# Kernel optimization log

Hardware: AMD Instinct MI355X
Metric: run time of the kernel (lower is better)

Reference implementation:

```python
import jax, jax.numpy as jnp
import numpy as np

B, F_IN, N, T = 32, 64, 512, 64


def setup_inputs() -> dict:
    key = jax.random.key(0)
    ks = jax.random.split(key, 6)
    s = 0.05  # small init scale so sigmoid/softmax stay in a sane range
    return {
        "x": jax.random.normal(ks[0], (B, F_IN, N, T), dtype=jnp.float32),
        "U1": jax.random.normal(ks[1], (N,), dtype=jnp.float32) * s,
        "U2": jax.random.normal(ks[2], (N, F_IN), dtype=jnp.float32) * s,
        "U3": jax.random.normal(ks[3], (F_IN,), dtype=jnp.float32) * s,
        "be": jax.random.normal(ks[4], (1, T, T), dtype=jnp.float32) * s,
        "Ve": jax.random.normal(ks[5], (T, T), dtype=jnp.float32) * s,
    }


def reference(x, U1, U2, U3, be, Ve):
    # x: (B, F, N, T)
    # lhs = U2 @ (x^T @ U1): (B, N, T)
    t1 = jnp.einsum("bfnt,n->bft", x, U1)          # (B, F, T)
    lhs = jnp.einsum("nf,bft->bnt", U2, t1)        # (B, N, T)
    # rhs = sum_f U3[f] * x[:, f]: (B, N, T)
    rhs = jnp.einsum("f,bfnt->bnt", U3, x)         # (B, N, T)
    # product = lhs^T @ rhs: (B, T, T)
    product = jnp.einsum("bnt,bns->bts", lhs, rhs)
    # E = Ve @ sigmoid(product + be): (B, T, T)
    E = jnp.einsum("ts,bsu->btu", Ve, jax.nn.sigmoid(product + be))
    # softmax over dim=1 (rows of E), then x_flat @ A, reshape back
    A = jax.nn.softmax(E, axis=1)                  # (B, T, T)
    out = jnp.einsum("bfnt,bts->bfns", x, A)       # (B, F, N, T)
    return out
```

## Files before the change

### kernel.cpp

```cpp
#include <hip/hip_runtime.h>
#include <hip/hip_bf16.h>

#define B_ 32
#define F_ 64
#define N_ 512
#define T_ 64

typedef __attribute__((ext_vector_type(8))) short bf16x8;
typedef __attribute__((ext_vector_type(4))) float f32x4;

__device__ __forceinline__ unsigned short f2bf(float f) {
  union { float f; unsigned int u; } v; v.f = f;
  unsigned int u = v.u;
  unsigned int r = (u + 0x7FFFu + ((u >> 16) & 1u)) >> 16;
  return (unsigned short)r;
}

__device__ __forceinline__ void gl_lds16(const float* g, float* l) {
  __builtin_amdgcn_global_load_lds(
      (const __attribute__((address_space(1))) unsigned int*)(g),
      (__attribute__((address_space(3))) unsigned int*)(l),
      16, 0, 0);
}

__global__ __launch_bounds__(256) void k1_reduce(const float* __restrict__ x,
    const float* __restrict__ U1, const float* __restrict__ U3,
    float* __restrict__ t1part, float* __restrict__ rhs) {
  const int b = blockIdx.x;
  const int nc = blockIdx.y;
  const int n0 = nc * 16;
  const int tid = threadIdx.x;
  const int w = tid >> 6;
  const int lane = tid & 63;
  const int n_sub = lane >> 4;
  const int t0 = (lane & 15) * 4;

  __shared__ float ring[4][2][1024];

  const float* fbase = x + ((size_t)(b * F_ + w * 16) * N_ + n0) * T_;

  float u1c[4];
#pragma unroll
  for (int i = 0; i < 4; ++i) u1c[i] = U1[n0 + n_sub * 4 + i];

  float racc[4][4];
#pragma unroll
  for (int i = 0; i < 4; ++i)
#pragma unroll
    for (int k = 0; k < 4; ++k) racc[i][k] = 0.f;

  {
    const float* s = fbase;
    float* l = &ring[w][0][0];
#pragma unroll
    for (int c = 0; c < 4; ++c) gl_lds16(s + c * 256 + lane * 4, l + c * 256);
  }

#pragma unroll 2
  for (int j = 0; j < 16; ++j) {
    const int buf = j & 1;
    if (j < 15) {
      const float* s = fbase + (size_t)(j + 1) * (N_ * T_);
      float* l = &ring[w][buf ^ 1][0];
#pragma unroll
      for (int c = 0; c < 4; ++c) gl_lds16(s + c * 256 + lane * 4, l + c * 256);
      asm volatile("s_waitcnt vmcnt(4)" ::: "memory");
    } else {
      asm volatile("s_waitcnt vmcnt(0)" ::: "memory");
    }
    __builtin_amdgcn_sched_barrier(0);

    const int f = w * 16 + j;
    const float u3 = U3[f];
    float p0 = 0.f, p1 = 0.f, p2 = 0.f, p3 = 0.f;
#pragma unroll
    for (int i = 0; i < 4; ++i) {
      const float4 v = *(const float4*)&ring[w][buf][(n_sub * 4 + i) * 64 + t0];
      racc[i][0] += u3 * v.x; racc[i][1] += u3 * v.y;
      racc[i][2] += u3 * v.z; racc[i][3] += u3 * v.w;
      p0 += u1c[i] * v.x; p1 += u1c[i] * v.y;
      p2 += u1c[i] * v.z; p3 += u1c[i] * v.w;
    }
    p0 += __shfl_xor(p0, 16); p0 += __shfl_xor(p0, 32);
    p1 += __shfl_xor(p1, 16); p1 += __shfl_xor(p1, 32);
    p2 += __shfl_xor(p2, 16); p2 += __shfl_xor(p2, 32);
    p3 += __shfl_xor(p3, 16); p3 += __shfl_xor(p3, 32);
    if (lane < 16) {
      float4 st; st.x = p0; st.y = p1; st.z = p2; st.w = p3;
      *(float4*)&t1part[((size_t)(b * 32 + nc) * 64 + f) * 64 + t0] = st;
    }
  }

#pragma unroll
  for (int i = 0; i < 4; ++i) {
    float4 st; st.x = racc[i][0]; st.y = racc[i][1]; st.z = racc[i][2]; st.w = racc[i][3];
    *(float4*)&ring[w][0][(n_sub * 4 + i) * 64 + t0] = st;
  }
  __syncthreads();
#pragma unroll
  for (int q = 0; q < 4; ++q) {
    const int idx = q * 256 + tid;
    const float s = ring[0][0][idx] + ring[1][0][idx] + ring[2][0][idx] + ring[3][0][idx];
    rhs[((size_t)b * N_ + n0 + (idx >> 6)) * T_ + (idx & 63)] = s;
  }
}

__global__ __launch_bounds__(256) void k2_w(const float* __restrict__ rhs,
    const float* __restrict__ U2, float* __restrict__ wpart) {
  const int b = blockIdx.x;
  const int c = blockIdx.y;
  const int n0 = c * 64;
  const int tid = threadIdx.x;
  const int s = tid & 63;
  const int fg = tid >> 6;
  __shared__ float lu2[64 * 64];
  __shared__ float lr[64 * 64];
#pragma unroll
  for (int q = 0; q < 16; ++q) {
    const int idx = q * 256 + tid;
    const int i = idx >> 6, cc = idx & 63;
    lu2[idx] = U2[(size_t)(n0 + i) * F_ + cc];
    lr[idx] = rhs[((size_t)b * N_ + n0 + i) * T_ + cc];
  }
  __syncthreads();
  float acc[16];
#pragma unroll
  for (int j = 0; j < 16; ++j) acc[j] = 0.f;
  for (int i = 0; i < 64; ++i) {
    const float rv = lr[i * 64 + s];
#pragma unroll
    for (int j = 0; j < 16; ++j) acc[j] += lu2[i * 64 + fg * 16 + j] * rv;
  }
#pragma unroll
  for (int j = 0; j < 16; ++j)
    wpart[(size_t)(b * 8 + c) * 4096 + (size_t)(fg * 16 + j) * 64 + s] = acc[j];
}

__global__ __launch_bounds__(256) void kred(const float* __restrict__ t1part,
    const float* __restrict__ wpart, float* __restrict__ t1, float* __restrict__ wbf) {
  const int gid = blockIdx.x * 256 + threadIdx.x;
  if (gid < 131072) {
    const int b = gid >> 12, idx = gid & 4095;
    const float* p = t1part + (size_t)b * 32 * 4096 + idx;
    float sum = 0.f;
#pragma unroll
    for (int c = 0; c < 32; ++c) sum += p[c * 4096];
    t1[gid] = sum;
  } else {
    const int g = gid - 131072;
    const int b = g >> 12, idx = g & 4095;
    const float* p = wpart + (size_t)b * 8 * 4096 + idx;
    float sum = 0.f;
#pragma unroll
    for (int c = 0; c < 8; ++c) sum += p[c * 4096];
    wbf[g] = sum;
  }
}

__global__ __launch_bounds__(256) void k3_attn(const float* __restrict__ t1,
    const float* __restrict__ wbuf, const float* __restrict__ be,
    const float* __restrict__ Ve, float* __restrict__ Amat) {
  const int b = blockIdx.x;
  const int tid = threadIdx.x;
  const int lane = tid & 63;
  const int tg = tid >> 6;
  __shared__ float bufA[64 * 65];
  __shared__ float bufB[64 * 65];
  __shared__ float red[2][4][64];
#pragma unroll
  for (int q = 0; q < 16; ++q) {
    const int idx = q * 256 + tid;
    const int r = idx >> 6, c = idx & 63;
    bufA[r * 65 + c] = t1[(size_t)b * 4096 + idx];
    bufB[r * 65 + c] = wbuf[(size_t)b * 4096 + idx];
  }
  __syncthreads();
  float prod[16];
#pragma unroll
  for (int j = 0; j < 16; ++j) prod[j] = 0.f;
  for (int f = 0; f < 64; ++f) {
    const float wv = bufB[f * 65 + lane];
#pragma unroll
    for (int j = 0; j < 16; ++j) prod[j] += bufA[f * 65 + tg * 16 + j] * wv;
  }
  __syncthreads();
#pragma unroll
  for (int j = 0; j < 16; ++j) {
    const int tt = tg * 16 + j;
    const float v = prod[j] + be[tt * 64 + lane];
    bufA[tt * 65 + lane] = 1.f / (1.f + __expf(-v));
  }
#pragma unroll
  for (int q = 0; q < 16; ++q) {
    const int idx = q * 256 + tid;
    bufB[(idx >> 6) * 65 + (idx & 63)] = Ve[idx];
  }
  __syncthreads();
  float E[16];
#pragma unroll
  for (int j = 0; j < 16; ++j) E[j] = 0.f;
  for (int s = 0; s < 64; ++s) {
    const float sv = bufA[s * 65 + lane];
#pragma unroll
    for (int j = 0; j < 16; ++j) E[j] += bufB[(tg * 16 + j) * 65 + s] * sv;
  }
  float m = E[0];
#pragma unroll
  for (int j = 1; j < 16; ++j) m = fmaxf(m, E[j]);
  red[0][tg][lane] = m;
  __syncthreads();
  m = fmaxf(fmaxf(red[0][0][lane], red[0][1][lane]),
            fmaxf(red[0][2][lane], red[0][3][lane]));
  float se = 0.f;
  float ex[16];
#pragma unroll
  for (int j = 0; j < 16; ++j) { ex[j] = __expf(E[j] - m); se += ex[j]; }
  red[1][tg][lane] = se;
  __syncthreads();
  const float gs = red[1][0][lane] + red[1][1][lane] + red[1][2][lane] + red[1][3][lane];
  const float inv = 1.f / gs;
#pragma unroll
  for (int j = 0; j < 16; ++j) {
    const int tt = tg * 16 + j;
    Amat[(size_t)b * 4096 + tt * 64 + lane] = ex[j] * inv;
  }
}

__global__ __launch_bounds__(256) void k4_out(const float* __restrict__ x,
    const float* __restrict__ Amat, float* __restrict__ out) {
  const int b = blockIdx.x;
  const int chunk = blockIdx.y;
  const int tid = threadIdx.x;
  const int wv = tid >> 6;
  const int l = tid & 63;
  __shared__ float lA[64 * 65];
  const float* Ab = Amat + (size_t)b * 4096;
#pragma unroll
  for (int q = 0; q < 16; ++q) {
    const int idx = q * 256 + tid;
    lA[(idx >> 6) * 65 + (idx & 63)] = Ab[idx];
  }
  __syncthreads();

  const int krow0 = (l >> 4) * 8;
  const int colb = l & 15;
  bf16x8 Bf[4][2];
#pragma unroll
  for (int nt = 0; nt < 4; ++nt)
#pragma unroll
    for (int kh = 0; kh < 2; ++kh) {
      bf16x8 fr;
#pragma unroll
      for (int j = 0; j < 8; ++j) {
        const int k = kh * 32 + krow0 + j;
        fr[j] = (short)f2bf(lA[k * 65 + nt * 16 + colb]);
      }
      Bf[nt][kh] = fr;
    }

  const float* Xb = x + (size_t)b * (F_ * (size_t)N_ * T_);
  float* Ob = out + (size_t)b * (F_ * (size_t)N_ * T_);
  const int rl = l & 15;
  const int c0 = (l >> 4) * 8;

  for (int it = 0; it < 4; ++it) {
    const int tile = chunk * 16 + wv * 4 + it;
    const int r = tile * 16 + rl;
    const float* xr = Xb + (size_t)r * T_;
    const float4 v0 = *(const float4*)(xr + c0);
    const float4 v1 = *(const float4*)(xr + c0 + 4);
    const float4 v2 = *(const float4*)(xr + 32 + c0);
    const float4 v3 = *(const float4*)(xr + 32 + c0 + 4);
    bf16x8 a0, a1;
    a0[0] = (short)f2bf(v0.x); a0[1] = (short)f2bf(v0.y);
    a0[2] = (short)f2bf(v0.z); a0[3] = (short)f2bf(v0.w);
    a0[4] = (short)f2bf(v1.x); a0[5] = (short)f2bf(v1.y);
    a0[6] = (short)f2bf(v1.z); a0[7] = (short)f2bf(v1.w);
    a1[0] = (short)f2bf(v2.x); a1[1] = (short)f2bf(v2.y);
    a1[2] = (short)f2bf(v2.z); a1[3] = (short)f2bf(v2.w);
    a1[4] = (short)f2bf(v3.x); a1[5] = (short)f2bf(v3.y);
    a1[6] = (short)f2bf(v3.z); a1[7] = (short)f2bf(v3.w);

    const int rowb = tile * 16 + (l >> 4) * 4;
#pragma unroll
    for (int nt = 0; nt < 4; ++nt) {
      f32x4 c = {0.f, 0.f, 0.f, 0.f};
      c = __builtin_amdgcn_mfma_f32_16x16x32_bf16(a0, Bf[nt][0], c, 0, 0, 0);
      c = __builtin_amdgcn_mfma_f32_16x16x32_bf16(a1, Bf[nt][1], c, 0, 0, 0);
#pragma unroll
      for (int j = 0; j < 4; ++j)
        Ob[(size_t)(rowb + j) * T_ + nt * 16 + colb] = c[j];
    }
  }
}

extern "C" void kernel_launch(void* const* d_in, const int* in_sizes, int n_in,
                              void* d_out, int out_size, void* d_ws, size_t ws_size,
                              hipStream_t stream) {
  const float* x  = (const float*)d_in[0];
  const float* U1 = (const float*)d_in[1];
  const float* U2 = (const float*)d_in[2];
  const float* U3 = (const float*)d_in[3];
  const float* be = (const float*)d_in[4];
  const float* Ve = (const float*)d_in[5];
  float* out = (float*)d_out;
  float* ws = (float*)d_ws;

  float* t1part = ws;
  float* rhs    = t1part + 4194304;
  float* wpart  = rhs + 1048576;
  float* t1     = wpart + 1048576;
  float* wbf    = t1 + 131072;
  float* Amat   = wbf + 131072;

  k1_reduce<<<dim3(32, 32), 256, 0, stream>>>(x, U1, U3, t1part, rhs);
  k2_w<<<dim3(32, 8), 256, 0, stream>>>(rhs, U2, wpart);
  kred<<<1024, 256, 0, stream>>>(t1part, wpart, t1, wbf);
  k3_attn<<<32, 256, 0, stream>>>(t1, wbf, be, Ve, Amat);
  k4_out<<<dim3(32, 128), 256, 0, stream>>>(x, Amat, out);
}
```

Measured before the change: 192.9 us.

## Widen k1 node tile to 64 with 4-slot LDS ring pipeline

Each k1_reduce block now covers 64 nodes instead of 16, so the grid drops from 32x32 to 32x8 blocks and the t1 partial buffer shrinks by a factor of four. The two-slot double buffer becomes a four-slot per-wave LDS ring that keeps three 4 KB loads in flight with vmcnt(12) waits. The goal is fewer partial writes, a cheaper kred reduction and deeper memory-level parallelism. The cost is far fewer blocks (256, so the x read may under-fill the GPU), 64 KB of LDS per block and more accumulator registers, which can lower occupancy.

```diff
diff --git a/kernel.cpp b/kernel.cpp
--- a/kernel.cpp
+++ b/kernel.cpp
@@ -28,58 +28,70 @@
     float* __restrict__ t1part, float* __restrict__ rhs) {
   const int b = blockIdx.x;
   const int nc = blockIdx.y;
-  const int n0 = nc * 16;
+  const int n0 = nc * 64;
   const int tid = threadIdx.x;
   const int w = tid >> 6;
   const int lane = tid & 63;
   const int n_sub = lane >> 4;
   const int t0 = (lane & 15) * 4;
 
-  __shared__ float ring[4][2][1024];
+  __shared__ float ring[4][4][1024];
 
   const float* fbase = x + ((size_t)(b * F_ + w * 16) * N_ + n0) * T_;
 
-  float u1c[4];
-#pragma unroll
-  for (int i = 0; i < 4; ++i) u1c[i] = U1[n0 + n_sub * 4 + i];
-
-  float racc[4][4];
-#pragma unroll
-  for (int i = 0; i < 4; ++i)
-#pragma unroll
-    for (int k = 0; k < 4; ++k) racc[i][k] = 0.f;
-
-  {
-    const float* s = fbase;
-    float* l = &ring[w][0][0];
+  float u1c[4][4];
+#pragma unroll
+  for (int m = 0; m < 4; ++m)
+#pragma unroll
+    for (int i = 0; i < 4; ++i) u1c[m][i] = U1[n0 + m * 16 + n_sub * 4 + i];
+
+  float racc[4][4][4];
+#pragma unroll
+  for (int m = 0; m < 4; ++m)
+#pragma unroll
+    for (int i = 0; i < 4; ++i)
+#pragma unroll
+      for (int k = 0; k < 4; ++k) racc[m][i][k] = 0.f;
+
+#pragma unroll
+  for (int s0 = 0; s0 < 3; ++s0) {
+    const float* s = fbase + s0 * 1024;
+    float* l = &ring[w][s0][0];
 #pragma unroll
     for (int c = 0; c < 4; ++c) gl_lds16(s + c * 256 + lane * 4, l + c * 256);
   }
 
-#pragma unroll 2
   for (int j = 0; j < 16; ++j) {
-    const int buf = j & 1;
-    if (j < 15) {
-      const float* s = fbase + (size_t)(j + 1) * (N_ * T_);
-      float* l = &ring[w][buf ^ 1][0];
-#pragma unroll
-      for (int c = 0; c < 4; ++c) gl_lds16(s + c * 256 + lane * 4, l + c * 256);
-      asm volatile("s_waitcnt vmcnt(4)" ::: "memory");
-    } else {
-      asm volatile("s_waitcnt vmcnt(0)" ::: "memory");
-    }
-    __builtin_amdgcn_sched_barrier(0);
-
-    const int f = w * 16 + j;
-    const float u3 = U3[f];
+    const float u3 = U3[w * 16 + j];
     float p0 = 0.f, p1 = 0.f, p2 = 0.f, p3 = 0.f;
 #pragma unroll
-    for (int i = 0; i < 4; ++i) {
-      const float4 v = *(const float4*)&ring[w][buf][(n_sub * 4 + i) * 64 + t0];
-      racc[i][0] += u3 * v.x; racc[i][1] += u3 * v.y;
-      racc[i][2] += u3 * v.z; racc[i][3] += u3 * v.w;
-      p0 += u1c[i] * v.x; p1 += u1c[i] * v.y;
-      p2 += u1c[i] * v.z; p3 += u1c[i] * v.w;
+    for (int m = 0; m < 4; ++m) {
+      if (j < 15 || m == 0) {
+        const int fp = (m == 0) ? j : (j + 1);
+        const int mp = (m + 3) & 3;
+        const float* s = fbase + (size_t)fp * (N_ * T_) + mp * 1024;
+        float* l = &ring[w][mp][0];
+#pragma unroll
+        for (int c = 0; c < 4; ++c) gl_lds16(s + c * 256 + lane * 4, l + c * 256);
+      }
+      if (j < 15) {
+        asm volatile("s_waitcnt vmcnt(12)" ::: "memory");
+      } else {
+        if (m == 0)      asm volatile("s_waitcnt vmcnt(12)" ::: "memory");
+        else if (m == 1) asm volatile("s_waitcnt vmcnt(8)"  ::: "memory");
+        else if (m == 2) asm volatile("s_waitcnt vmcnt(4)"  ::: "memory");
+        else             asm volatile("s_waitcnt vmcnt(0)"  ::: "memory");
+      }
+      __builtin_amdgcn_sched_barrier(0);
+
+#pragma unroll
+      for (int i = 0; i < 4; ++i) {
+        const float4 v = *(const float4*)&ring[w][m][(n_sub * 4 + i) * 64 + t0];
+        racc[m][i][0] += u3 * v.x; racc[m][i][1] += u3 * v.y;
+        racc[m][i][2] += u3 * v.z; racc[m][i][3] += u3 * v.w;
+        p0 += u1c[m][i] * v.x; p1 += u1c[m][i] * v.y;
+        p2 += u1c[m][i] * v.z; p3 += u1c[m][i] * v.w;
+      }
     }
     p0 += __shfl_xor(p0, 16); p0 += __shfl_xor(p0, 32);
     p1 += __shfl_xor(p1, 16); p1 += __shfl_xor(p1, 32);
@@ -87,20 +99,24 @@
     p3 += __shfl_xor(p3, 16); p3 += __shfl_xor(p3, 32);
     if (lane < 16) {
       float4 st; st.x = p0; st.y = p1; st.z = p2; st.w = p3;
-      *(float4*)&t1part[((size_t)(b * 32 + nc) * 64 + f) * 64 + t0] = st;
-    }
-  }
-
-#pragma unroll
-  for (int i = 0; i < 4; ++i) {
-    float4 st; st.x = racc[i][0]; st.y = racc[i][1]; st.z = racc[i][2]; st.w = racc[i][3];
-    *(float4*)&ring[w][0][(n_sub * 4 + i) * 64 + t0] = st;
-  }
-  __syncthreads();
-#pragma unroll
-  for (int q = 0; q < 4; ++q) {
-    const int idx = q * 256 + tid;
-    const float s = ring[0][0][idx] + ring[1][0][idx] + ring[2][0][idx] + ring[3][0][idx];
+      *(float4*)&t1part[((size_t)(b * 8 + nc) * 64 + (w * 16 + j)) * 64 + t0] = st;
+    }
+  }
+
+#pragma unroll
+  for (int m = 0; m < 4; ++m)
+#pragma unroll
+    for (int i = 0; i < 4; ++i) {
+      float4 st; st.x = racc[m][i][0]; st.y = racc[m][i][1];
+      st.z = racc[m][i][2]; st.w = racc[m][i][3];
+      *(float4*)&ring[w][0][(m * 16 + n_sub * 4 + i) * 64 + t0] = st;
+    }
+  __syncthreads();
+  const float* r0 = &ring[0][0][0];
+#pragma unroll
+  for (int q = 0; q < 16; ++q) {
+    const int idx = q * 256 + tid;
+    const float s = r0[idx] + r0[4096 + idx] + r0[8192 + idx] + r0[12288 + idx];
     rhs[((size_t)b * N_ + n0 + (idx >> 6)) * T_ + (idx & 63)] = s;
   }
 }
@@ -141,10 +157,10 @@
   const int gid = blockIdx.x * 256 + threadIdx.x;
   if (gid < 131072) {
     const int b = gid >> 12, idx = gid & 4095;
-    const float* p = t1part + (size_t)b * 32 * 4096 + idx;
+    const float* p = t1part + (size_t)b * 8 * 4096 + idx;
     float sum = 0.f;
 #pragma unroll
-    for (int c = 0; c < 32; ++c) sum += p[c * 4096];
+    for (int c = 0; c < 8; ++c) sum += p[c * 4096];
     t1[gid] = sum;
   } else {
     const int g = gid - 131072;
@@ -307,13 +323,13 @@
   float* ws = (float*)d_ws;
 
   float* t1part = ws;
-  float* rhs    = t1part + 4194304;
+  float* rhs    = t1part + 1048576;
   float* wpart  = rhs + 1048576;
   float* t1     = wpart + 1048576;
   float* wbf    = t1 + 131072;
   float* Amat   = wbf + 131072;
 
-  k1_reduce<<<dim3(32, 32), 256, 0, stream>>>(x, U1, U3, t1part, rhs);
+  k1_reduce<<<dim3(32, 8), 256, 0, stream>>>(x, U1, U3, t1part, rhs);
   k2_w<<<dim3(32, 8), 256, 0, stream>>>(rhs, U2, wpart);
   kred<<<1024, 256, 0, stream>>>(t1part, wpart, t1, wbf);
   k3_attn<<<32, 256, 0, stream>>>(t1, wbf, be, Ve, Amat);
```

Measured after the change: 191.8 us. Within noise of the previous version (-0.6%).
